# Optimization experiments

Hardware: AMD Instinct MI355X
Metric: run time of the kernel (lower is better)

The kernel has to match this reference:

```python
import jax, jax.numpy as jnp
import numpy as np

B, D, H = 8192, 1024, 1024


def setup_inputs() -> dict:
    key = jax.random.key(0)
    k = jax.random.split(key, 6)
    s_x = 1.0 / np.sqrt(D)
    s_h = 1.0 / np.sqrt(H)
    return {
        "x": jax.random.normal(k[0], (B, D), dtype=jnp.float32),
        "h_prev": jax.random.normal(k[1], (B, H), dtype=jnp.float32),
        "c_prev": jax.random.normal(k[2], (B, H), dtype=jnp.float32),
        # Stacked gate weights in order [i, f, o, g] (exactly equivalent to
        # the 8 separate nn.Linear layers, fused into 2 GEMMs).
        "Wx": jax.random.uniform(k[3], (4 * H, D), jnp.float32, -s_x, s_x),
        "Wh": jax.random.uniform(k[4], (4 * H, H), jnp.float32, -s_h, s_h),
        # combined bias of W_* and U_* linears per gate
        "b": jax.random.uniform(k[5], (4 * H,), jnp.float32, -s_x, s_x),
    }


def reference(x, h_prev, c_prev, Wx, Wh, b):
    # gates: [B, 4H], gate order i, f, o, g
    gates = x @ Wx.T + h_prev @ Wh.T + b
    i, f, o, g = jnp.split(gates, 4, axis=-1)
    c_t = jax.nn.sigmoid(f) * c_prev + jax.nn.sigmoid(i) * jnp.tanh(g)
    h_t = jax.nn.sigmoid(o) * jnp.tanh(c_t)
    return (h_t, c_t)
```

## Files before the change

kernel.cpp:

```cpp
#include <hip/hip_runtime.h>
#include <hip/hip_bf16.h>
#include <stdint.h>

#define B_ROWS 8192
#define D_DIM  1024
#define H_DIM  1024
#define K_DIM  2048
#define N_GATES 4096

#define BM 128
#define BN 64
#define BK 64

#define KC (K_DIM / 32)
#define A_M16 (B_ROWS / 16)
#define W_N16 (N_GATES / 16)
#define A_CHUNKS (A_M16 * KC)
#define W_CHUNKS (W_N16 * KC)
#define A_WS_BYTES ((size_t)A_CHUNKS * 1024)
#define W_WS_BYTES ((size_t)W_CHUNKS * 1024)

#define TBM 256
#define TBH 64
#define NT  KC
#define NBUF 4

typedef __bf16 bf16x8 __attribute__((ext_vector_type(8)));
typedef float  f32x4  __attribute__((ext_vector_type(4)));
using bf16_t = __hip_bfloat16;

__device__ __forceinline__ float sigm(float x) {
  return 1.0f / (1.0f + __expf(-x));
}
__device__ __forceinline__ float tanh_fast(float x) {
  return 1.0f - 2.0f / (__expf(2.0f * x) + 1.0f);
}

__device__ __forceinline__ void async_ld16(const void* g, void* l) {
  __builtin_amdgcn_global_load_lds(
      (const __attribute__((address_space(1))) unsigned int*)g,
      (__attribute__((address_space(3))) unsigned int*)l, 16, 0, 0);
}

__global__ void pack_tiles(const float* __restrict__ x,
                           const float* __restrict__ h,
                           const float* __restrict__ Wx,
                           const float* __restrict__ Wh,
                           bf16_t* __restrict__ aws,
                           bf16_t* __restrict__ wws) {
  const int wave = threadIdx.x >> 6, lane = threadIdx.x & 63;
  int c = blockIdx.x * 4 + wave;
  const int r16 = lane & 15, quad = lane >> 4;
  const float* src;
  size_t soff;
  bf16_t* dst;
  if (c < A_CHUNKS) {
    const int m16 = c / KC, k32 = c % KC;
    const int k = k32 * 32 + quad * 8;
    src = (k < D_DIM) ? x : h;
    soff = (size_t)(m16 * 16 + r16) * 1024 + (k & 1023);
    dst = aws + (size_t)c * 512;
  } else {
    c -= A_CHUNKS;
    const int n16 = c / KC, k32 = c % KC;
    const int k = k32 * 32 + quad * 8;
    src = (k < D_DIM) ? Wx : Wh;
    soff = (size_t)(n16 * 16 + r16) * 1024 + (k & 1023);
    dst = wws + (size_t)c * 512;
  }
  const f32x4 a = *(const f32x4*)(src + soff);
  const f32x4 b = *(const f32x4*)(src + soff + 4);
  bf16x8 v;
#pragma unroll
  for (int i = 0; i < 4; ++i) { v[i] = (__bf16)a[i]; v[i + 4] = (__bf16)b[i]; }
  *(bf16x8*)(dst + lane * 8) = v;
}

__global__ __launch_bounds__(512, 2) void lstm_mfma(
    const bf16_t* __restrict__ aws, const bf16_t* __restrict__ wws,
    const float* __restrict__ c_prev, const float* __restrict__ bias,
    float* __restrict__ h_out, float* __restrict__ c_out) {
  __shared__ __align__(16) bf16_t sA[NBUF * 16 * 512];
  __shared__ __align__(16) bf16_t sB[NBUF * 16 * 512];

  const int tid  = threadIdx.x;
  const int wave = tid >> 6;
  const int lane = tid & 63;

  const int xcd = blockIdx.x & 7;
  const int idx = blockIdx.x >> 3;
  const int m_blk = (xcd >> 1) * 8 + (idx & 7);
  const int n_blk = (xcd & 1) * 8 + (idx >> 3);
  const int m0 = m_blk * TBM;
  const int n0 = n_blk * TBH;
  const int m16_0 = m0 >> 4;
  const int n16_0 = n0 >> 4;

  const int wm = wave >> 2;
  const int wh = wave & 3;
  const int lr = lane & 15, quad = lane >> 4;

  f32x4 acc[4][8];
#pragma unroll
  for (int g = 0; g < 4; ++g)
#pragma unroll
    for (int mi = 0; mi < 8; ++mi) {
      f32x4 z = {0.0f, 0.0f, 0.0f, 0.0f};
      acc[g][mi] = z;
    }

  auto stageA = [&](int half, int tt, int pb) {
    const int mi = half * 8 + wave;
    const bf16_t* g = aws + ((size_t)(m16_0 + mi) * KC + tt) * 512 + lane * 8;
    bf16_t* l = sA + ((pb * 16 + mi) * 512) + lane * 8;
    async_ld16(g, l);
  };
  auto stageB = [&](int half, int tt, int pb) {
    const int j = half * 8 + wave;
    const int n16 = (j >> 2) * (H_DIM / 16) + n16_0 + (j & 3);
    const bf16_t* g = wws + ((size_t)n16 * KC + tt) * 512 + lane * 8;
    bf16_t* l = sB + ((pb * 16 + j) * 512) + lane * 8;
    async_ld16(g, l);
  };

  stageA(0, 0, 0); stageA(1, 0, 0); stageB(0, 0, 0); stageB(1, 0, 0);
  stageA(0, 1, 1); stageA(1, 1, 1); stageB(0, 1, 1); stageB(1, 1, 1);
  stageA(0, 2, 2); stageA(1, 2, 2); stageB(0, 2, 2); stageB(1, 2, 2);
  asm volatile("s_waitcnt vmcnt(8)" ::: "memory");
  __builtin_amdgcn_s_barrier();

  for (int t = 0; t < NT; ++t) {
    const int cur = t & 3;
    const int pf  = (t + 3) & 3;
    const bf16_t* bufA = sA + cur * (16 * 512);
    const bf16_t* bufB = sB + cur * (16 * 512);
    const bool pre = (t + 3 < NT);

    bf16x8 af[4], bw[4];
#pragma unroll
    for (int x = 0; x < 4; ++x)
      af[x] = *(const bf16x8*)&bufA[(wm * 8 + x) * 512 + lane * 8];
#pragma unroll
    for (int g = 0; g < 4; ++g)
      bw[g] = *(const bf16x8*)&bufB[(g * 4 + wh) * 512 + lane * 8];
    if (pre) { stageA(0, t + 3, pf); stageA(1, t + 3, pf); }
    asm volatile("" ::: "memory");
    __builtin_amdgcn_s_barrier();
    asm volatile("s_waitcnt lgkmcnt(0)" ::: "memory");
    __builtin_amdgcn_sched_barrier(0);
    __builtin_amdgcn_s_setprio(1);
#pragma unroll
    for (int g = 0; g < 4; ++g)
#pragma unroll
      for (int x = 0; x < 4; ++x)
        acc[g][x] = __builtin_amdgcn_mfma_f32_16x16x32_bf16(
            af[x], bw[g], acc[g][x], 0, 0, 0);
    __builtin_amdgcn_s_setprio(0);
    asm volatile("" ::: "memory");
    __builtin_amdgcn_s_barrier();

#pragma unroll
    for (int x = 0; x < 4; ++x)
      af[x] = *(const bf16x8*)&bufA[(wm * 8 + 4 + x) * 512 + lane * 8];
    if (pre) { stageB(0, t + 3, pf); stageB(1, t + 3, pf); }
    if (t + 3 < NT)      asm volatile("s_waitcnt vmcnt(8)" ::: "memory");
    else if (t + 2 < NT) asm volatile("s_waitcnt vmcnt(4)" ::: "memory");
    else if (t + 1 < NT) asm volatile("s_waitcnt vmcnt(0)" ::: "memory");
    asm volatile("" ::: "memory");
    __builtin_amdgcn_s_barrier();
    asm volatile("s_waitcnt lgkmcnt(0)" ::: "memory");
    __builtin_amdgcn_sched_barrier(0);
    __builtin_amdgcn_s_setprio(1);
#pragma unroll
    for (int g = 0; g < 4; ++g)
#pragma unroll
      for (int x = 0; x < 4; ++x)
        acc[g][4 + x] = __builtin_amdgcn_mfma_f32_16x16x32_bf16(
            af[x], bw[g], acc[g][4 + x], 0, 0, 0);
    __builtin_amdgcn_s_setprio(0);
    asm volatile("" ::: "memory");
    __builtin_amdgcn_s_barrier();
  }

  const int col = n0 + wh * 16 + lr;
  const float bi  = bias[col];
  const float bfv = bias[H_DIM + col];
  const float bo  = bias[2 * H_DIM + col];
  const float bg  = bias[3 * H_DIM + col];
#pragma unroll
  for (int mi = 0; mi < 8; ++mi) {
#pragma unroll
    for (int r = 0; r < 4; ++r) {
      const int m = m0 + wm * 128 + mi * 16 + quad * 4 + r;
      const size_t off = (size_t)m * H_DIM + col;
      const float iv = acc[0][mi][r] + bi;
      const float fv = acc[1][mi][r] + bfv;
      const float ov = acc[2][mi][r] + bo;
      const float gv = acc[3][mi][r] + bg;
      const float cp = c_prev[off];
      const float ct = sigm(fv) * cp + sigm(iv) * tanh_fast(gv);
      h_out[off] = sigm(ov) * tanh_fast(ct);
      c_out[off] = ct;
    }
  }
}

__device__ __forceinline__ int sw_(int row, int chunk) {
  return row * BK + ((chunk ^ (row & 7)) << 3);
}

__global__ __launch_bounds__(256, 2) void lstm_f32(
    const float* __restrict__ x, const float* __restrict__ h_prev,
    const float* __restrict__ c_prev, const float* __restrict__ Wx,
    const float* __restrict__ Wh, const float* __restrict__ bias,
    float* __restrict__ h_out, float* __restrict__ c_out) {
  __shared__ bf16_t sA[BM * BK];
  __shared__ bf16_t sB[4 * BN * BK];
  const int tid = threadIdx.x, wave = tid >> 6, lane = tid & 63;
  const int m0 = blockIdx.x * BM, n0 = blockIdx.y * BN;
  const int wm = wave >> 1, wn = wave & 1;
  const int lr = lane & 15, quad = lane >> 4;
  f32x4 acc[4][4][2];
#pragma unroll
  for (int g = 0; g < 4; ++g)
#pragma unroll
    for (int ti = 0; ti < 4; ++ti)
#pragma unroll
      for (int tj = 0; tj < 2; ++tj) {
        f32x4 z = {0.0f, 0.0f, 0.0f, 0.0f};
        acc[g][ti][tj] = z;
      }
  const int srow = lane >> 3, lc = lane & 7, scol = lc << 3;
  for (int k0 = 0; k0 < K_DIM; k0 += BK) {
    const float* aSrc; const float* wSrc; int kh;
    if (k0 < D_DIM) { aSrc = x; wSrc = Wx; kh = k0; }
    else            { aSrc = h_prev; wSrc = Wh; kh = k0 - D_DIM; }
    f32x4 stg[12][2];
#pragma unroll
    for (int t = 0; t < 12; ++t) {
      const int chunk = wave + t * 4;
      const float* g;
      if (chunk < 16) {
        g = aSrc + (size_t)(m0 + chunk * 8 + srow) * 1024 + kh + scol;
      } else {
        const int j = chunk - 16;
        g = wSrc + (size_t)((j >> 3) * H_DIM + n0 + (j & 7) * 8 + srow) * 1024 + kh + scol;
      }
      stg[t][0] = *(const f32x4*)g;
      stg[t][1] = *(const f32x4*)(g + 4);
    }
    __syncthreads();
#pragma unroll
    for (int t = 0; t < 12; ++t) {
      const int chunk = wave + t * 4;
      bf16x8 v;
#pragma unroll
      for (int i = 0; i < 4; ++i) {
        v[i] = (__bf16)stg[t][0][i];
        v[i + 4] = (__bf16)stg[t][1][i];
      }
      bf16_t* dst;
      if (chunk < 16) dst = &sA[sw_(chunk * 8 + srow, lc)];
      else {
        const int j = chunk - 16;
        dst = &sB[(j >> 3) * (BN * BK) + sw_((j & 7) * 8 + srow, lc)];
      }
      *(bf16x8*)dst = v;
    }
    __syncthreads();
#pragma unroll
    for (int kk = 0; kk < BK; kk += 32) {
      const int cbase = kk >> 3;
      bf16x8 af[4];
#pragma unroll
      for (int ti = 0; ti < 4; ++ti)
        af[ti] = *(const bf16x8*)&sA[sw_(wm * 64 + ti * 16 + lr, cbase + quad)];
      bf16x8 bw[4][2];
#pragma unroll
      for (int g = 0; g < 4; ++g)
#pragma unroll
        for (int tj = 0; tj < 2; ++tj)
          bw[g][tj] = *(const bf16x8*)
              &sB[g * (BN * BK) + sw_(wn * 32 + tj * 16 + lr, cbase + quad)];
#pragma unroll
      for (int g = 0; g < 4; ++g)
#pragma unroll
        for (int ti = 0; ti < 4; ++ti)
#pragma unroll
          for (int tj = 0; tj < 2; ++tj)
            acc[g][ti][tj] = __builtin_amdgcn_mfma_f32_16x16x32_bf16(
                af[ti], bw[g][tj], acc[g][ti][tj], 0, 0, 0);
    }
  }
#pragma unroll
  for (int tj = 0; tj < 2; ++tj) {
    const int n = n0 + wn * 32 + tj * 16 + lr;
    const float bi = bias[n], bf = bias[H_DIM + n];
    const float bo = bias[2 * H_DIM + n], bg = bias[3 * H_DIM + n];
#pragma unroll
    for (int ti = 0; ti < 4; ++ti)
#pragma unroll
      for (int r = 0; r < 4; ++r) {
        const int m = m0 + wm * 64 + ti * 16 + quad * 4 + r;
        const size_t off = (size_t)m * H_DIM + n;
        const float iv = acc[0][ti][tj][r] + bi;
        const float fv = acc[1][ti][tj][r] + bf;
        const float ov = acc[2][ti][tj][r] + bo;
        const float gv = acc[3][ti][tj][r] + bg;
        const float cp = c_prev[off];
        const float ct = sigm(fv) * cp + sigm(iv) * tanh_fast(gv);
        h_out[off] = sigm(ov) * tanh_fast(ct);
        c_out[off] = ct;
      }
  }
}

extern "C" void kernel_launch(void* const* d_in, const int* in_sizes, int n_in,
                              void* d_out, int out_size, void* d_ws, size_t ws_size,
                              hipStream_t stream) {
  const float* x      = (const float*)d_in[0];
  const float* h_prev = (const float*)d_in[1];
  const float* c_prev = (const float*)d_in[2];
  const float* Wx     = (const float*)d_in[3];
  const float* Wh     = (const float*)d_in[4];
  const float* b      = (const float*)d_in[5];
  float* h_out = (float*)d_out;
  float* c_out = (float*)d_out + (size_t)B_ROWS * H_DIM;

  if (ws_size >= A_WS_BYTES + W_WS_BYTES) {
    bf16_t* aws = (bf16_t*)d_ws;
    bf16_t* wws = (bf16_t*)((char*)d_ws + A_WS_BYTES);
    pack_tiles<<<(A_CHUNKS + W_CHUNKS) / 4, 256, 0, stream>>>(x, h_prev, Wx, Wh,
                                                              aws, wws);
    const int nblk = (B_ROWS / TBM) * (H_DIM / TBH);
    lstm_mfma<<<nblk, 512, 0, stream>>>(aws, wws, c_prev, b, h_out, c_out);
  } else {
    dim3 grid(B_ROWS / BM, H_DIM / BN, 1);
    lstm_f32<<<grid, 256, 0, stream>>>(x, h_prev, c_prev, Wx, Wh, b, h_out, c_out);
  }
}
```

Before: 297.7 us.

## Software-pipeline LDS fragment loads across k-tiles with ping-pong registers

Restructures the main GEMM loop so the LDS fragment reads for the next k-tile are issued before the current MFMA block, using ping-pong register sets and a loop unrolled by two. Global pointers are precomputed once, so per-stage address math is smaller. The vmcnt wait thresholds and barrier placement change, and the explicit lgkmcnt waits and sched_barriers are removed. The aim is to hide LDS latency behind MFMAs, at the cost of more VGPRs and reliance on compiler-inserted waits for correctness.

```diff
diff --git a/kernel.cpp b/kernel.cpp
--- a/kernel.cpp
+++ b/kernel.cpp
@@ -24,6 +24,7 @@
 #define TBH 64
 #define NT  KC
 #define NBUF 4
+#define SBUF (16 * 512)
 
 typedef __bf16 bf16x8 __attribute__((ext_vector_type(8)));
 typedef float  f32x4  __attribute__((ext_vector_type(4)));
@@ -41,6 +42,9 @@
       (const __attribute__((address_space(1))) unsigned int*)g,
       (__attribute__((address_space(3))) unsigned int*)l, 16, 0, 0);
 }
+
+#define FENCE() asm volatile("" ::: "memory")
+#define BAR() do { FENCE(); __builtin_amdgcn_s_barrier(); FENCE(); } while (0)
 
 __global__ void pack_tiles(const float* __restrict__ x,
                            const float* __restrict__ h,
@@ -80,8 +84,8 @@
     const bf16_t* __restrict__ aws, const bf16_t* __restrict__ wws,
     const float* __restrict__ c_prev, const float* __restrict__ bias,
     float* __restrict__ h_out, float* __restrict__ c_out) {
-  __shared__ __align__(16) bf16_t sA[NBUF * 16 * 512];
-  __shared__ __align__(16) bf16_t sB[NBUF * 16 * 512];
+  __shared__ __align__(16) bf16_t sA[NBUF * SBUF];
+  __shared__ __align__(16) bf16_t sB[NBUF * SBUF];
 
   const int tid  = threadIdx.x;
   const int wave = tid >> 6;
@@ -109,77 +113,82 @@
       acc[g][mi] = z;
     }
 
-  auto stageA = [&](int half, int tt, int pb) {
-    const int mi = half * 8 + wave;
-    const bf16_t* g = aws + ((size_t)(m16_0 + mi) * KC + tt) * 512 + lane * 8;
-    bf16_t* l = sA + ((pb * 16 + mi) * 512) + lane * 8;
-    async_ld16(g, l);
-  };
-  auto stageB = [&](int half, int tt, int pb) {
-    const int j = half * 8 + wave;
-    const int n16 = (j >> 2) * (H_DIM / 16) + n16_0 + (j & 3);
-    const bf16_t* g = wws + ((size_t)n16 * KC + tt) * 512 + lane * 8;
-    bf16_t* l = sB + ((pb * 16 + j) * 512) + lane * 8;
-    async_ld16(g, l);
-  };
-
-  stageA(0, 0, 0); stageA(1, 0, 0); stageB(0, 0, 0); stageB(1, 0, 0);
-  stageA(0, 1, 1); stageA(1, 1, 1); stageB(0, 1, 1); stageB(1, 1, 1);
-  stageA(0, 2, 2); stageA(1, 2, 2); stageB(0, 2, 2); stageB(1, 2, 2);
+  const bf16_t* gA  = aws + (size_t)(m16_0 + wave) * KC * 512 + lane * 8;
+  const bf16_t* gA8 = gA + (size_t)8 * KC * 512;
+  const int n16w = (wave >> 2) * (H_DIM / 16) + n16_0 + (wave & 3);
+  const bf16_t* gB  = wws + (size_t)n16w * KC * 512 + lane * 8;
+  const bf16_t* gB8 = gB + (size_t)128 * KC * 512;
+  bf16_t* lA  = sA + wave * 512 + lane * 8;
+  bf16_t* lA8 = lA + 8 * 512;
+  bf16_t* lB  = sB + wave * 512 + lane * 8;
+  bf16_t* lB8 = lB + 8 * 512;
+
+  auto STAGE_A = [&](int tt) {
+    const int bo = (tt & 3) * SBUF;
+    const size_t go = (size_t)tt * 512;
+    async_ld16(gA + go, lA + bo);
+    async_ld16(gA8 + go, lA8 + bo);
+  };
+  auto STAGE_B = [&](int tt) {
+    const int bo = (tt & 3) * SBUF;
+    const size_t go = (size_t)tt * 512;
+    async_ld16(gB + go, lB + bo);
+    async_ld16(gB8 + go, lB8 + bo);
+  };
+
+  const int rA = wm * 8 * 512 + lane * 8;
+  const int rB = wh * 512 + lane * 8;
+
+  auto LD_AF = [&](bf16x8 (&dst)[4], int bufo, int half4) {
+#pragma unroll
+    for (int x = 0; x < 4; ++x)
+      dst[x] = *(const bf16x8*)&sA[bufo + rA + (half4 + x) * 512];
+  };
+  auto LD_BW = [&](bf16x8 (&dst)[4], int bufo) {
+#pragma unroll
+    for (int g = 0; g < 4; ++g)
+      dst[g] = *(const bf16x8*)&sB[bufo + rB + g * 4 * 512];
+  };
+  auto MMA = [&](const bf16x8 (&a)[4], const bf16x8 (&b)[4], int s) {
+    __builtin_amdgcn_s_setprio(1);
+#pragma unroll
+    for (int g = 0; g < 4; ++g)
+#pragma unroll
+      for (int x = 0; x < 4; ++x)
+        acc[g][s + x] = __builtin_amdgcn_mfma_f32_16x16x32_bf16(
+            a[x], b[g], acc[g][s + x], 0, 0, 0);
+    __builtin_amdgcn_s_setprio(0);
+  };
+
+  STAGE_A(0); STAGE_B(0); STAGE_A(1); STAGE_B(1); STAGE_A(2); STAGE_B(2);
   asm volatile("s_waitcnt vmcnt(8)" ::: "memory");
-  __builtin_amdgcn_s_barrier();
-
-  for (int t = 0; t < NT; ++t) {
-    const int cur = t & 3;
-    const int pf  = (t + 3) & 3;
-    const bf16_t* bufA = sA + cur * (16 * 512);
-    const bf16_t* bufB = sB + cur * (16 * 512);
-    const bool pre = (t + 3 < NT);
-
-    bf16x8 af[4], bw[4];
-#pragma unroll
-    for (int x = 0; x < 4; ++x)
-      af[x] = *(const bf16x8*)&bufA[(wm * 8 + x) * 512 + lane * 8];
-#pragma unroll
-    for (int g = 0; g < 4; ++g)
-      bw[g] = *(const bf16x8*)&bufB[(g * 4 + wh) * 512 + lane * 8];
-    if (pre) { stageA(0, t + 3, pf); stageA(1, t + 3, pf); }
-    asm volatile("" ::: "memory");
-    __builtin_amdgcn_s_barrier();
-    asm volatile("s_waitcnt lgkmcnt(0)" ::: "memory");
-    __builtin_amdgcn_sched_barrier(0);
-    __builtin_amdgcn_s_setprio(1);
-#pragma unroll
-    for (int g = 0; g < 4; ++g)
-#pragma unroll
-      for (int x = 0; x < 4; ++x)
-        acc[g][x] = __builtin_amdgcn_mfma_f32_16x16x32_bf16(
-            af[x], bw[g], acc[g][x], 0, 0, 0);
-    __builtin_amdgcn_s_setprio(0);
-    asm volatile("" ::: "memory");
-    __builtin_amdgcn_s_barrier();
-
-#pragma unroll
-    for (int x = 0; x < 4; ++x)
-      af[x] = *(const bf16x8*)&bufA[(wm * 8 + 4 + x) * 512 + lane * 8];
-    if (pre) { stageB(0, t + 3, pf); stageB(1, t + 3, pf); }
-    if (t + 3 < NT)      asm volatile("s_waitcnt vmcnt(8)" ::: "memory");
+  BAR();
+
+  bf16x8 afA[4], bwA[4], afB[4], bwB[4];
+  LD_AF(afA, 0, 0);
+  LD_BW(bwA, 0);
+
+  auto tile_step = [&](int t, bf16x8 (&afc)[4], bf16x8 (&bwc)[4],
+                       bf16x8 (&afn)[4], bf16x8 (&bwn)[4]) {
+    const int cbo = (t & 3) * SBUF;
+    const int nbo = ((t + 1) & 3) * SBUF;
+    bf16x8 af2[4];
+    LD_AF(af2, cbo, 4);
+    if (t + 3 < NT) STAGE_A(t + 3);
+    MMA(afc, bwc, 0);
+    if (t + 3 < NT)      asm volatile("s_waitcnt vmcnt(6)" ::: "memory");
     else if (t + 2 < NT) asm volatile("s_waitcnt vmcnt(4)" ::: "memory");
     else if (t + 1 < NT) asm volatile("s_waitcnt vmcnt(0)" ::: "memory");
-    asm volatile("" ::: "memory");
-    __builtin_amdgcn_s_barrier();
-    asm volatile("s_waitcnt lgkmcnt(0)" ::: "memory");
-    __builtin_amdgcn_sched_barrier(0);
-    __builtin_amdgcn_s_setprio(1);
-#pragma unroll
-    for (int g = 0; g < 4; ++g)
-#pragma unroll
-      for (int x = 0; x < 4; ++x)
-        acc[g][4 + x] = __builtin_amdgcn_mfma_f32_16x16x32_bf16(
-            af[x], bw[g], acc[g][4 + x], 0, 0, 0);
-    __builtin_amdgcn_s_setprio(0);
-    asm volatile("" ::: "memory");
-    __builtin_amdgcn_s_barrier();
+    BAR();
+    if (t + 1 < NT) { LD_AF(afn, nbo, 0); LD_BW(bwn, nbo); }
+    if (t + 3 < NT) STAGE_B(t + 3);
+    MMA(af2, bwc, 4);
+    BAR();
+  };
+
+  for (int t = 0; t < NT; t += 2) {
+    tile_step(t,     afA, bwA, afB, bwB);
+    tile_step(t + 1, afB, bwB, afA, bwA);
   }
 
   const int col = n0 + wh * 16 + lr;
```

Measured after the change: 306.5 us. +3.0%, slower.
